# Kernel optimization log

Measured on AMD Instinct MI355X. Metric: run time of the kernel, lower is better.

The kernel has to match this reference:

```python
import jax, jax.numpy as jnp
import numpy as np

N, D, C, P = 4096, 512, 100, 64
EPS_COS = 1e-8   # torch cosine_similarity norm clamp
EPS_INV = 1e-5   # module's 1/(d + 1e-5)


def setup_inputs() -> dict:
    key = jax.random.key(0)
    k1, k2, k3, k4 = jax.random.split(key, 4)
    feats = jax.random.normal(k1, (N, D), dtype=jnp.float32)
    protos = jax.random.normal(k2, (C, P, D), dtype=jnp.float32)
    cls_ids = jax.random.randint(k3, (N,), 0, C)
    proto_labels = jax.random.randint(k4, (C, P), 0, 1000)
    return {"feats": feats, "protos": protos, "cls_ids": cls_ids,
            "proto_labels": proto_labels}


def reference(feats, protos, cls_ids, proto_labels):
    # Gather each box's class-conditional prototype set: [N, P, D]
    p = protos[cls_ids]
    pl = proto_labels[cls_ids]                       # [N, P]

    # cosine distance: 1 - f.p / (max(|f|,eps) * max(|p|,eps))
    dot = jnp.einsum('nd,npd->np', feats, p)         # [N, P]
    fnorm = jnp.maximum(jnp.linalg.norm(feats, axis=-1, keepdims=True), EPS_COS)
    pnorm = jnp.maximum(jnp.linalg.norm(p, axis=-1), EPS_COS)
    d_cos = 1.0 - dot / (fnorm * pnorm)

    diff = feats[:, None, :] - p                     # [N, P, D]
    d_l1 = jnp.mean(jnp.abs(diff), axis=-1)          # F.l1_loss (mean)
    d_l2 = jnp.mean(diff * diff, axis=-1)            # F.mse_loss (mean)

    dists = jnp.stack([d_cos, d_l1, d_l2], axis=1)   # [N, 3, P]
    probs = jax.nn.softmax(1.0 / (dists + EPS_INV), axis=-1).mean(axis=1)  # [N, P]

    idx = jnp.argmax(probs, axis=-1)                 # [N]
    labels = jnp.take_along_axis(pl, idx[:, None], axis=1)[:, 0]
    return labels, probs
```

## Files before the change

kernel.cpp:

```cpp
#include <hip/hip_runtime.h>

#define D 512
#define P 64
#define WPB 4
#define EPS_COS 1e-8f
#define EPS_INV 1e-5f

__device__ __forceinline__ float wave_sum(float v) {
#pragma unroll
    for (int m = 32; m >= 1; m >>= 1) v += __shfl_xor(v, m, 64);
    return v;
}

__global__ __launch_bounds__(256) void proto_norm_kernel(
    const float* __restrict__ protos, float* __restrict__ pp, int rows)
{
    const int lane = threadIdx.x & 63;
    const int wave = threadIdx.x >> 6;
    const int r = blockIdx.x * WPB + wave;
    if (r >= rows) return;
    const float* row = protos + (size_t)r * D;
    const float4 a = *(const float4*)(row + lane * 4);
    const float4 b = *(const float4*)(row + 256 + lane * 4);
    float s = a.x*a.x + a.y*a.y + a.z*a.z + a.w*a.w
            + b.x*b.x + b.y*b.y + b.z*b.z + b.w*b.w;
    s = wave_sum(s);
    if (lane == 0) pp[r] = s;
}

__global__ __launch_bounds__(WPB * 64) void proto_probs_kernel(
    const float* __restrict__ feats,
    const float* __restrict__ protos,
    const int*   __restrict__ cls_ids,
    const int*   __restrict__ proto_labels,
    const float* __restrict__ ppbuf,
    float* __restrict__ out,
    int N)
{
    const int lane = threadIdx.x & 63;
    const int wave = threadIdx.x >> 6;
    const int n = blockIdx.x * WPB + wave;
    if (n >= N) return;

    const int cls = cls_ids[n];
    const float* f  = feats  + (size_t)n * D;
    const float* pr = protos + (size_t)cls * (P * D);

    const float4 f0 = *(const float4*)(f + lane * 4);
    const float4 f1 = *(const float4*)(f + 256 + lane * 4);

    float ff = f0.x*f0.x + f0.y*f0.y + f0.z*f0.z + f0.w*f0.w
             + f1.x*f1.x + f1.y*f1.y + f1.z*f1.z + f1.w*f1.w;
    ff = wave_sum(ff);

    const int jsel = (lane >> 3) & 7;
    const int gown = lane & 7;
    const bool hi32 = (lane & 32) != 0;
    const bool hi16 = (lane & 16) != 0;
    const bool hi8  = (lane & 8)  != 0;

    float r_dot = 0.f, r_l1 = 0.f;

    for (int g = 0; g < 8; ++g) {
        float pd[8], pl[8];
#pragma unroll
        for (int j = 0; j < 8; ++j) {
            const float* row = pr + (size_t)(8 * g + j) * D;
            const float4 q0 = *(const float4*)(row + lane * 4);
            const float4 q1 = *(const float4*)(row + 256 + lane * 4);
            float dot, l1, t;
            dot  = f0.x*q0.x; t = f0.x - q0.x; l1  = fabsf(t);
            dot += f0.y*q0.y; t = f0.y - q0.y; l1 += fabsf(t);
            dot += f0.z*q0.z; t = f0.z - q0.z; l1 += fabsf(t);
            dot += f0.w*q0.w; t = f0.w - q0.w; l1 += fabsf(t);
            dot += f1.x*q1.x; t = f1.x - q1.x; l1 += fabsf(t);
            dot += f1.y*q1.y; t = f1.y - q1.y; l1 += fabsf(t);
            dot += f1.z*q1.z; t = f1.z - q1.z; l1 += fabsf(t);
            dot += f1.w*q1.w; t = f1.w - q1.w; l1 += fabsf(t);
            pd[j] = dot; pl[j] = l1;
        }
#pragma unroll
        for (int k = 0; k < 4; ++k) {
            const float sd = hi32 ? pd[k] : pd[k + 4];
            const float sl = hi32 ? pl[k] : pl[k + 4];
            const float rd = __shfl_xor(sd, 32, 64);
            const float rl = __shfl_xor(sl, 32, 64);
            pd[k] = (hi32 ? pd[k + 4] : pd[k]) + rd;
            pl[k] = (hi32 ? pl[k + 4] : pl[k]) + rl;
        }
#pragma unroll
        for (int k = 0; k < 2; ++k) {
            const float sd = hi16 ? pd[k] : pd[k + 2];
            const float sl = hi16 ? pl[k] : pl[k + 2];
            const float rd = __shfl_xor(sd, 16, 64);
            const float rl = __shfl_xor(sl, 16, 64);
            pd[k] = (hi16 ? pd[k + 2] : pd[k]) + rd;
            pl[k] = (hi16 ? pl[k + 2] : pl[k]) + rl;
        }
        {
            const float sd = hi8 ? pd[0] : pd[1];
            const float sl = hi8 ? pl[0] : pl[1];
            const float rd = __shfl_xor(sd, 8, 64);
            const float rl = __shfl_xor(sl, 8, 64);
            pd[0] = (hi8 ? pd[1] : pd[0]) + rd;
            pl[0] = (hi8 ? pl[1] : pl[0]) + rl;
        }
#pragma unroll
        for (int m = 4; m >= 1; m >>= 1) {
            pd[0] += __shfl_xor(pd[0], m, 64);
            pl[0] += __shfl_xor(pl[0], m, 64);
        }
        if (gown == g) { r_dot = pd[0]; r_l1 = pl[0]; }
    }

    const int myp = 8 * gown + jsel;
    const float s_pp = ppbuf[cls * P + myp];

    const float fnorm = fmaxf(sqrtf(ff),   EPS_COS);
    const float pnorm = fmaxf(sqrtf(s_pp), EPS_COS);
    const float d_cos = 1.0f - r_dot / (fnorm * pnorm);
    const float d_l1  = r_l1 * (1.0f / (float)D);
    const float d_l2  = (ff - 2.0f * r_dot + s_pp) * (1.0f / (float)D);

    float s[3];
    s[0] = 1.0f / (d_cos + EPS_INV);
    s[1] = 1.0f / (d_l1  + EPS_INV);
    s[2] = 1.0f / (d_l2  + EPS_INV);

    float prob = 0.f;
#pragma unroll
    for (int i = 0; i < 3; ++i) {
        float m = s[i];
#pragma unroll
        for (int w = 32; w >= 1; w >>= 1) m = fmaxf(m, __shfl_xor(m, w, 64));
        const float e = expf(s[i] - m);
        const float denom = wave_sum(e);
        prob += e / denom;
    }
    prob *= (1.0f / 3.0f);

    float best = prob;
    int   bidx = myp;
#pragma unroll
    for (int w = 32; w >= 1; w >>= 1) {
        const float ov = __shfl_xor(best, w, 64);
        const int   oi = __shfl_xor(bidx, w, 64);
        if (ov > best || (ov == best && oi < bidx)) { best = ov; bidx = oi; }
    }

    out[(size_t)N + (size_t)n * P + myp] = prob;
    if (lane == 0) {
        out[n] = (float)proto_labels[cls * P + bidx];
    }
}

extern "C" void kernel_launch(void* const* d_in, const int* in_sizes, int n_in,
                              void* d_out, int out_size, void* d_ws, size_t ws_size,
                              hipStream_t stream) {
    const float* feats        = (const float*)d_in[0];
    const float* protos       = (const float*)d_in[1];
    const int*   cls_ids      = (const int*)d_in[2];
    const int*   proto_labels = (const int*)d_in[3];
    float* out = (float*)d_out;
    float* pp  = (float*)d_ws;

    const int N    = in_sizes[2];
    const int rows = in_sizes[1] / D;

    proto_norm_kernel<<<(rows + WPB - 1) / WPB, WPB * 64, 0, stream>>>(
        protos, pp, rows);
    proto_probs_kernel<<<(N + WPB - 1) / WPB, WPB * 64, 0, stream>>>(
        feats, protos, cls_ids, proto_labels, pp, out, N);
}
```

Before: 104.6 us.

## Group boxes by class so each wave reuses prototype loads for two boxes

```diff
diff --git a/kernel.cpp b/kernel.cpp
--- a/kernel.cpp
+++ b/kernel.cpp
@@ -3,6 +3,8 @@
 #define D 512
 #define P 64
 #define WPB 4
+#define NB 2
+#define MAXC 256
 #define EPS_COS 1e-8f
 #define EPS_INV 1e-5f
 
@@ -28,30 +30,117 @@
     if (lane == 0) pp[r] = s;
 }
 
+__global__ __launch_bounds__(1024) void build_groups_kernel(
+    const int* __restrict__ cls_ids, int* __restrict__ slots,
+    int* __restrict__ gcount, int N, int C)
+{
+    __shared__ int cnt[MAXC], base[MAXC], fill[MAXC];
+    __shared__ int sG;
+    const int tid = threadIdx.x;
+    for (int c = tid; c < C; c += 1024) { cnt[c] = 0; fill[c] = 0; }
+    __syncthreads();
+    for (int n = tid; n < N; n += 1024) atomicAdd(&cnt[cls_ids[n]], 1);
+    __syncthreads();
+    if (tid == 0) {
+        int gb = 0;
+        for (int c = 0; c < C; ++c) { base[c] = gb; gb += (cnt[c] + NB - 1) / NB; }
+        sG = gb;
+        gcount[0] = gb;
+    }
+    __syncthreads();
+    const int G = sG;
+    for (int i = tid; i < G * NB; i += 1024) slots[i] = -1;
+    __syncthreads();
+    for (int n = tid; n < N; n += 1024) {
+        const int c = cls_ids[n];
+        const int p = atomicAdd(&fill[c], 1);
+        slots[base[c] * NB + p] = n;
+    }
+}
+
+__device__ __forceinline__ void box_epilogue(
+    float r_dot, float r_l1, float ff, float s_pp, int myp,
+    float& prob_o, int& bidx_o)
+{
+    const float fnorm = fmaxf(sqrtf(ff),   EPS_COS);
+    const float pnorm = fmaxf(sqrtf(s_pp), EPS_COS);
+    const float d_cos = 1.0f - r_dot / (fnorm * pnorm);
+    const float d_l1  = r_l1 * (1.0f / (float)D);
+    const float d_l2  = (ff - 2.0f * r_dot + s_pp) * (1.0f / (float)D);
+
+    float s[3];
+    s[0] = 1.0f / (d_cos + EPS_INV);
+    s[1] = 1.0f / (d_l1  + EPS_INV);
+    s[2] = 1.0f / (d_l2  + EPS_INV);
+
+    float prob = 0.f;
+#pragma unroll
+    for (int i = 0; i < 3; ++i) {
+        float m = s[i];
+#pragma unroll
+        for (int w = 32; w >= 1; w >>= 1) m = fmaxf(m, __shfl_xor(m, w, 64));
+        const float e = expf(s[i] - m);
+        const float denom = wave_sum(e);
+        prob += e / denom;
+    }
+    prob *= (1.0f / 3.0f);
+
+    float best = prob;
+    int   bidx = myp;
+#pragma unroll
+    for (int w = 32; w >= 1; w >>= 1) {
+        const float ov = __shfl_xor(best, w, 64);
+        const int   oi = __shfl_xor(bidx, w, 64);
+        if (ov > best || (ov == best && oi < bidx)) { best = ov; bidx = oi; }
+    }
+    prob_o = prob;
+    bidx_o = bidx;
+}
+
 __global__ __launch_bounds__(WPB * 64) void proto_probs_kernel(
     const float* __restrict__ feats,
     const float* __restrict__ protos,
     const int*   __restrict__ cls_ids,
     const int*   __restrict__ proto_labels,
     const float* __restrict__ ppbuf,
+    const int*   __restrict__ slots,
+    const int*   __restrict__ gcount,
     float* __restrict__ out,
     int N)
 {
     const int lane = threadIdx.x & 63;
     const int wave = threadIdx.x >> 6;
-    const int n = blockIdx.x * WPB + wave;
-    if (n >= N) return;
-
-    const int cls = cls_ids[n];
-    const float* f  = feats  + (size_t)n * D;
+
+    const int nb  = gridDim.x;
+    const int q   = nb >> 3, r = nb & 7;
+    const int xcd = blockIdx.x & 7, bix = blockIdx.x >> 3;
+    const int swz = (xcd < r ? xcd * (q + 1) : r * (q + 1) + (xcd - r) * q) + bix;
+
+    const int g = swz * WPB + wave;
+    if (g >= gcount[0]) return;
+
+    const int b0 = slots[g * NB + 0];
+    const int b1 = slots[g * NB + 1];
+    const bool v1 = (b1 >= 0);
+    const int n0 = b0;
+    const int n1 = v1 ? b1 : b0;
+
+    const int cls = cls_ids[n0];
+    const float* fa = feats  + (size_t)n0 * D;
+    const float* fb = feats  + (size_t)n1 * D;
     const float* pr = protos + (size_t)cls * (P * D);
 
-    const float4 f0 = *(const float4*)(f + lane * 4);
-    const float4 f1 = *(const float4*)(f + 256 + lane * 4);
-
-    float ff = f0.x*f0.x + f0.y*f0.y + f0.z*f0.z + f0.w*f0.w
-             + f1.x*f1.x + f1.y*f1.y + f1.z*f1.z + f1.w*f1.w;
-    ff = wave_sum(ff);
+    const float4 a0 = *(const float4*)(fa + lane * 4);
+    const float4 a1 = *(const float4*)(fa + 256 + lane * 4);
+    const float4 c0 = *(const float4*)(fb + lane * 4);
+    const float4 c1 = *(const float4*)(fb + 256 + lane * 4);
+
+    float ffa = a0.x*a0.x + a0.y*a0.y + a0.z*a0.z + a0.w*a0.w
+              + a1.x*a1.x + a1.y*a1.y + a1.z*a1.z + a1.w*a1.w;
+    float ffb = c0.x*c0.x + c0.y*c0.y + c0.z*c0.z + c0.w*c0.w
+              + c1.x*c1.x + c1.y*c1.y + c1.z*c1.z + c1.w*c1.w;
+    ffa = wave_sum(ffa);
+    ffb = wave_sum(ffb);
 
     const int jsel = (lane >> 3) & 7;
     const int gown = lane & 7;
@@ -59,98 +148,101 @@
     const bool hi16 = (lane & 16) != 0;
     const bool hi8  = (lane & 8)  != 0;
 
-    float r_dot = 0.f, r_l1 = 0.f;
-
-    for (int g = 0; g < 8; ++g) {
-        float pd[8], pl[8];
+    float rdA = 0.f, rlA = 0.f, rdB = 0.f, rlB = 0.f;
+
+    for (int gg = 0; gg < 8; ++gg) {
+        float pdA[8], plA[8], pdB[8], plB[8];
 #pragma unroll
         for (int j = 0; j < 8; ++j) {
-            const float* row = pr + (size_t)(8 * g + j) * D;
+            const float* row = pr + (size_t)(8 * gg + j) * D;
             const float4 q0 = *(const float4*)(row + lane * 4);
             const float4 q1 = *(const float4*)(row + 256 + lane * 4);
-            float dot, l1, t;
-            dot  = f0.x*q0.x; t = f0.x - q0.x; l1  = fabsf(t);
-            dot += f0.y*q0.y; t = f0.y - q0.y; l1 += fabsf(t);
-            dot += f0.z*q0.z; t = f0.z - q0.z; l1 += fabsf(t);
-            dot += f0.w*q0.w; t = f0.w - q0.w; l1 += fabsf(t);
-            dot += f1.x*q1.x; t = f1.x - q1.x; l1 += fabsf(t);
-            dot += f1.y*q1.y; t = f1.y - q1.y; l1 += fabsf(t);
-            dot += f1.z*q1.z; t = f1.z - q1.z; l1 += fabsf(t);
-            dot += f1.w*q1.w; t = f1.w - q1.w; l1 += fabsf(t);
-            pd[j] = dot; pl[j] = l1;
+            float dA, lA, dB, lB, t;
+            dA  = a0.x*q0.x; t = a0.x - q0.x; lA  = fabsf(t);
+            dA += a0.y*q0.y; t = a0.y - q0.y; lA += fabsf(t);
+            dA += a0.z*q0.z; t = a0.z - q0.z; lA += fabsf(t);
+            dA += a0.w*q0.w; t = a0.w - q0.w; lA += fabsf(t);
+            dA += a1.x*q1.x; t = a1.x - q1.x; lA += fabsf(t);
+            dA += a1.y*q1.y; t = a1.y - q1.y; lA += fabsf(t);
+            dA += a1.z*q1.z; t = a1.z - q1.z; lA += fabsf(t);
+            dA += a1.w*q1.w; t = a1.w - q1.w; lA += fabsf(t);
+            dB  = c0.x*q0.x; t = c0.x - q0.x; lB  = fabsf(t);
+            dB += c0.y*q0.y; t = c0.y - q0.y; lB += fabsf(t);
+            dB += c0.z*q0.z; t = c0.z - q0.z; lB += fabsf(t);
+            dB += c0.w*q0.w; t = c0.w - q0.w; lB += fabsf(t);
+            dB += c1.x*q1.x; t = c1.x - q1.x; lB += fabsf(t);
+            dB += c1.y*q1.y; t = c1.y - q1.y; lB += fabsf(t);
+            dB += c1.z*q1.z; t = c1.z - q1.z; lB += fabsf(t);
+            dB += c1.w*q1.w; t = c1.w - q1.w; lB += fabsf(t);
+            pdA[j] = dA; plA[j] = lA; pdB[j] = dB; plB[j] = lB;
         }
 #pragma unroll
         for (int k = 0; k < 4; ++k) {
-            const float sd = hi32 ? pd[k] : pd[k + 4];
-            const float sl = hi32 ? pl[k] : pl[k + 4];
-            const float rd = __shfl_xor(sd, 32, 64);
-            const float rl = __shfl_xor(sl, 32, 64);
-            pd[k] = (hi32 ? pd[k + 4] : pd[k]) + rd;
-            pl[k] = (hi32 ? pl[k + 4] : pl[k]) + rl;
+            const float sdA = hi32 ? pdA[k] : pdA[k + 4];
+            const float slA = hi32 ? plA[k] : plA[k + 4];
+            const float sdB = hi32 ? pdB[k] : pdB[k + 4];
+            const float slB = hi32 ? plB[k] : plB[k + 4];
+            const float rd0 = __shfl_xor(sdA, 32, 64);
+            const float rl0 = __shfl_xor(slA, 32, 64);
+            const float rd1 = __shfl_xor(sdB, 32, 64);
+            const float rl1 = __shfl_xor(slB, 32, 64);
+            pdA[k] = (hi32 ? pdA[k + 4] : pdA[k]) + rd0;
+            plA[k] = (hi32 ? plA[k + 4] : plA[k]) + rl0;
+            pdB[k] = (hi32 ? pdB[k + 4] : pdB[k]) + rd1;
+            plB[k] = (hi32 ? plB[k + 4] : plB[k]) + rl1;
         }
 #pragma unroll
         for (int k = 0; k < 2; ++k) {
-            const float sd = hi16 ? pd[k] : pd[k + 2];
-            const float sl = hi16 ? pl[k] : pl[k + 2];
-            const float rd = __shfl_xor(sd, 16, 64);
-            const float rl = __shfl_xor(sl, 16, 64);
-            pd[k] = (hi16 ? pd[k + 2] : pd[k]) + rd;
-            pl[k] = (hi16 ? pl[k + 2] : pl[k]) + rl;
+            const float sdA = hi16 ? pdA[k] : pdA[k + 2];
+            const float slA = hi16 ? plA[k] : plA[k + 2];
+            const float sdB = hi16 ? pdB[k] : pdB[k + 2];
+            const float slB = hi16 ? plB[k] : plB[k + 2];
+            const float rd0 = __shfl_xor(sdA, 16, 64);
+            const float rl0 = __shfl_xor(slA, 16, 64);
+            const float rd1 = __shfl_xor(sdB, 16, 64);
+            const float rl1 = __shfl_xor(slB, 16, 64);
+            pdA[k] = (hi16 ? pdA[k + 2] : pdA[k]) + rd0;
+            plA[k] = (hi16 ? plA[k + 2] : plA[k]) + rl0;
+            pdB[k] = (hi16 ? pdB[k + 2] : pdB[k]) + rd1;
+            plB[k] = (hi16 ? plB[k + 2] : plB[k]) + rl1;
         }
         {
-            const float sd = hi8 ? pd[0] : pd[1];
-            const float sl = hi8 ? pl[0] : pl[1];
-            const float rd = __shfl_xor(sd, 8, 64);
-            const float rl = __shfl_xor(sl, 8, 64);
-            pd[0] = (hi8 ? pd[1] : pd[0]) + rd;
-            pl[0] = (hi8 ? pl[1] : pl[0]) + rl;
+            const float sdA = hi8 ? pdA[0] : pdA[1];
+            const float slA = hi8 ? plA[0] : plA[1];
+            const float sdB = hi8 ? pdB[0] : pdB[1];
+            const float slB = hi8 ? plB[0] : plB[1];
+            const float rd0 = __shfl_xor(sdA, 8, 64);
+            const float rl0 = __shfl_xor(slA, 8, 64);
+            const float rd1 = __shfl_xor(sdB, 8, 64);
+            const float rl1 = __shfl_xor(slB, 8, 64);
+            pdA[0] = (hi8 ? pdA[1] : pdA[0]) + rd0;
+            plA[0] = (hi8 ? plA[1] : plA[0]) + rl0;
+            pdB[0] = (hi8 ? pdB[1] : pdB[0]) + rd1;
+            plB[0] = (hi8 ? plB[1] : plB[0]) + rl1;
         }
 #pragma unroll
         for (int m = 4; m >= 1; m >>= 1) {
-            pd[0] += __shfl_xor(pd[0], m, 64);
-            pl[0] += __shfl_xor(pl[0], m, 64);
-        }
-        if (gown == g) { r_dot = pd[0]; r_l1 = pl[0]; }
+            pdA[0] += __shfl_xor(pdA[0], m, 64);
+            plA[0] += __shfl_xor(plA[0], m, 64);
+            pdB[0] += __shfl_xor(pdB[0], m, 64);
+            plB[0] += __shfl_xor(plB[0], m, 64);
+        }
+        if (gown == gg) { rdA = pdA[0]; rlA = plA[0]; rdB = pdB[0]; rlB = plB[0]; }
     }
 
     const int myp = 8 * gown + jsel;
     const float s_pp = ppbuf[cls * P + myp];
 
-    const float fnorm = fmaxf(sqrtf(ff),   EPS_COS);
-    const float pnorm = fmaxf(sqrtf(s_pp), EPS_COS);
-    const float d_cos = 1.0f - r_dot / (fnorm * pnorm);
-    const float d_l1  = r_l1 * (1.0f / (float)D);
-    const float d_l2  = (ff - 2.0f * r_dot + s_pp) * (1.0f / (float)D);
-
-    float s[3];
-    s[0] = 1.0f / (d_cos + EPS_INV);
-    s[1] = 1.0f / (d_l1  + EPS_INV);
-    s[2] = 1.0f / (d_l2  + EPS_INV);
-
-    float prob = 0.f;
-#pragma unroll
-    for (int i = 0; i < 3; ++i) {
-        float m = s[i];
-#pragma unroll
-        for (int w = 32; w >= 1; w >>= 1) m = fmaxf(m, __shfl_xor(m, w, 64));
-        const float e = expf(s[i] - m);
-        const float denom = wave_sum(e);
-        prob += e / denom;
-    }
-    prob *= (1.0f / 3.0f);
-
-    float best = prob;
-    int   bidx = myp;
-#pragma unroll
-    for (int w = 32; w >= 1; w >>= 1) {
-        const float ov = __shfl_xor(best, w, 64);
-        const int   oi = __shfl_xor(bidx, w, 64);
-        if (ov > best || (ov == best && oi < bidx)) { best = ov; bidx = oi; }
-    }
-
-    out[(size_t)N + (size_t)n * P + myp] = prob;
-    if (lane == 0) {
-        out[n] = (float)proto_labels[cls * P + bidx];
+    float probA; int bidxA;
+    box_epilogue(rdA, rlA, ffa, s_pp, myp, probA, bidxA);
+    out[(size_t)N + (size_t)n0 * P + myp] = probA;
+    if (lane == 0) out[n0] = (float)proto_labels[cls * P + bidxA];
+
+    if (v1) {
+        float probB; int bidxB;
+        box_epilogue(rdB, rlB, ffb, s_pp, myp, probB, bidxB);
+        out[(size_t)N + (size_t)n1 * P + myp] = probB;
+        if (lane == 0) out[n1] = (float)proto_labels[cls * P + bidxB];
     }
 }
 
@@ -162,13 +254,21 @@
     const int*   cls_ids      = (const int*)d_in[2];
     const int*   proto_labels = (const int*)d_in[3];
     float* out = (float*)d_out;
-    float* pp  = (float*)d_ws;
 
     const int N    = in_sizes[2];
     const int rows = in_sizes[1] / D;
+    const int C    = rows / P;
+
+    float* pp     = (float*)d_ws;
+    int*   gcount = (int*)((char*)d_ws + (size_t)rows * sizeof(float));
+    int*   slots  = gcount + 1;
+
+    const int Gmax    = (N + C * (NB - 1)) / NB;
+    const int mblocks = (Gmax + WPB - 1) / WPB;
 
     proto_norm_kernel<<<(rows + WPB - 1) / WPB, WPB * 64, 0, stream>>>(
         protos, pp, rows);
-    proto_probs_kernel<<<(N + WPB - 1) / WPB, WPB * 64, 0, stream>>>(
-        feats, protos, cls_ids, proto_labels, pp, out, N);
-}
+    build_groups_kernel<<<1, 1024, 0, stream>>>(cls_ids, slots, gcount, N, C);
+    proto_probs_kernel<<<mblocks, WPB * 64, 0, stream>>>(
+        feats, protos, cls_ids, proto_labels, pp, slots, gcount, out, N);
+}
```

Measured after the change: 119.2 us. +14.0%, slower.

## Group boxes by class in pairs, transpose prototypes, one prototype per lane

Applied to the files above, without the earlier changes.

```diff
diff --git a/kernel.cpp b/kernel.cpp
--- a/kernel.cpp
+++ b/kernel.cpp
@@ -1,8 +1,11 @@
 #include <hip/hip_runtime.h>
 
 #define D 512
+#define D4 (D / 4)
 #define P 64
 #define WPB 4
+#define NB 2
+#define MAXC 256
 #define EPS_COS 1e-8f
 #define EPS_INV 1e-5f
 
@@ -12,145 +15,183 @@
     return v;
 }
 
-__global__ __launch_bounds__(256) void proto_norm_kernel(
-    const float* __restrict__ protos, float* __restrict__ pp, int rows)
+__global__ __launch_bounds__(256) void prep_kernel(
+    const float* __restrict__ protos, float* __restrict__ pp,
+    float* __restrict__ protosT, int rows,
+    const int* __restrict__ cls_ids, int* __restrict__ slots,
+    int* __restrict__ gcount, int N, int C, int normBlocks, int trBlocks)
 {
+    const int bid  = blockIdx.x;
     const int lane = threadIdx.x & 63;
     const int wave = threadIdx.x >> 6;
-    const int r = blockIdx.x * WPB + wave;
-    if (r >= rows) return;
-    const float* row = protos + (size_t)r * D;
-    const float4 a = *(const float4*)(row + lane * 4);
-    const float4 b = *(const float4*)(row + 256 + lane * 4);
-    float s = a.x*a.x + a.y*a.y + a.z*a.z + a.w*a.w
-            + b.x*b.x + b.y*b.y + b.z*b.z + b.w*b.w;
-    s = wave_sum(s);
-    if (lane == 0) pp[r] = s;
+
+    if (bid < normBlocks) {
+        const int r = bid * WPB + wave;
+        if (r >= rows) return;
+        const float* row = protos + (size_t)r * D;
+        const float4 a = *(const float4*)(row + lane * 4);
+        const float4 b = *(const float4*)(row + 256 + lane * 4);
+        float s = a.x*a.x + a.y*a.y + a.z*a.z + a.w*a.w
+                + b.x*b.x + b.y*b.y + b.z*b.z + b.w*b.w;
+        s = wave_sum(s);
+        if (lane == 0) pp[r] = s;
+        return;
+    }
+
+    if (bid < normBlocks + trBlocks) {
+        const int idx = (bid - normBlocks) * WPB + wave;
+        if (idx >= C * D4) return;
+        const int c  = idx >> 7;
+        const int d4 = idx & (D4 - 1);
+        const float4 v = *(const float4*)(protos + (size_t)(c * P + lane) * D + 4 * d4);
+        *(float4*)(protosT + ((size_t)(c * D4 + d4) * P + lane) * 4) = v;
+        return;
+    }
+
+    __shared__ int cnt[MAXC], bas[MAXC], fil[MAXC];
+    __shared__ int sv[256];
+    const int tid = threadIdx.x;
+    for (int c = tid; c < MAXC; c += 256) { cnt[c] = 0; fil[c] = 0; }
+    __syncthreads();
+    for (int n = tid; n < N; n += 256) atomicAdd(&cnt[cls_ids[n]], 1);
+    __syncthreads();
+    int v = 0;
+    if (tid < C) v = (cnt[tid] + NB - 1) / NB;
+    sv[tid] = v;
+    __syncthreads();
+#pragma unroll
+    for (int off = 1; off < 256; off <<= 1) {
+        const int t = (tid >= off) ? sv[tid - off] : 0;
+        __syncthreads();
+        sv[tid] += t;
+        __syncthreads();
+    }
+    const int G = sv[255];
+    if (tid < C) bas[tid] = sv[tid] - v;
+    if (tid == 0) gcount[0] = G;
+    __syncthreads();
+    for (int i = tid; i < G * NB; i += 256) slots[i] = -1;
+    __syncthreads();
+    for (int n = tid; n < N; n += 256) {
+        const int c = cls_ids[n];
+        const int p = atomicAdd(&fil[c], 1);
+        slots[bas[c] * NB + p] = n;
+    }
+}
+
+__device__ __forceinline__ void box_epilogue(
+    float r_dot, float r_l1, float ff, float s_pp, int myp,
+    float& prob_o, int& bidx_o)
+{
+    const float fnorm = fmaxf(sqrtf(ff),   EPS_COS);
+    const float pnorm = fmaxf(sqrtf(s_pp), EPS_COS);
+    const float d_cos = 1.0f - r_dot / (fnorm * pnorm);
+    const float d_l1  = r_l1 * (1.0f / (float)D);
+    const float d_l2  = (ff - 2.0f * r_dot + s_pp) * (1.0f / (float)D);
+
+    float s[3];
+    s[0] = 1.0f / (d_cos + EPS_INV);
+    s[1] = 1.0f / (d_l1  + EPS_INV);
+    s[2] = 1.0f / (d_l2  + EPS_INV);
+
+    float prob = 0.f;
+#pragma unroll
+    for (int i = 0; i < 3; ++i) {
+        float m = s[i];
+#pragma unroll
+        for (int w = 32; w >= 1; w >>= 1) m = fmaxf(m, __shfl_xor(m, w, 64));
+        const float e = expf(s[i] - m);
+        const float denom = wave_sum(e);
+        prob += e / denom;
+    }
+    prob *= (1.0f / 3.0f);
+
+    float best = prob;
+    int   bidx = myp;
+#pragma unroll
+    for (int w = 32; w >= 1; w >>= 1) {
+        const float ov = __shfl_xor(best, w, 64);
+        const int   oi = __shfl_xor(bidx, w, 64);
+        if (ov > best || (ov == best && oi < bidx)) { best = ov; bidx = oi; }
+    }
+    prob_o = prob;
+    bidx_o = bidx;
 }
 
 __global__ __launch_bounds__(WPB * 64) void proto_probs_kernel(
     const float* __restrict__ feats,
-    const float* __restrict__ protos,
+    const float* __restrict__ protosT,
     const int*   __restrict__ cls_ids,
     const int*   __restrict__ proto_labels,
     const float* __restrict__ ppbuf,
+    const int*   __restrict__ slots,
+    const int*   __restrict__ gcount,
     float* __restrict__ out,
     int N)
 {
     const int lane = threadIdx.x & 63;
     const int wave = threadIdx.x >> 6;
-    const int n = blockIdx.x * WPB + wave;
-    if (n >= N) return;
-
-    const int cls = cls_ids[n];
-    const float* f  = feats  + (size_t)n * D;
-    const float* pr = protos + (size_t)cls * (P * D);
-
-    const float4 f0 = *(const float4*)(f + lane * 4);
-    const float4 f1 = *(const float4*)(f + 256 + lane * 4);
-
-    float ff = f0.x*f0.x + f0.y*f0.y + f0.z*f0.z + f0.w*f0.w
-             + f1.x*f1.x + f1.y*f1.y + f1.z*f1.z + f1.w*f1.w;
-    ff = wave_sum(ff);
-
-    const int jsel = (lane >> 3) & 7;
-    const int gown = lane & 7;
-    const bool hi32 = (lane & 32) != 0;
-    const bool hi16 = (lane & 16) != 0;
-    const bool hi8  = (lane & 8)  != 0;
-
-    float r_dot = 0.f, r_l1 = 0.f;
-
-    for (int g = 0; g < 8; ++g) {
-        float pd[8], pl[8];
-#pragma unroll
-        for (int j = 0; j < 8; ++j) {
-            const float* row = pr + (size_t)(8 * g + j) * D;
-            const float4 q0 = *(const float4*)(row + lane * 4);
-            const float4 q1 = *(const float4*)(row + 256 + lane * 4);
-            float dot, l1, t;
-            dot  = f0.x*q0.x; t = f0.x - q0.x; l1  = fabsf(t);
-            dot += f0.y*q0.y; t = f0.y - q0.y; l1 += fabsf(t);
-            dot += f0.z*q0.z; t = f0.z - q0.z; l1 += fabsf(t);
-            dot += f0.w*q0.w; t = f0.w - q0.w; l1 += fabsf(t);
-            dot += f1.x*q1.x; t = f1.x - q1.x; l1 += fabsf(t);
-            dot += f1.y*q1.y; t = f1.y - q1.y; l1 += fabsf(t);
-            dot += f1.z*q1.z; t = f1.z - q1.z; l1 += fabsf(t);
-            dot += f1.w*q1.w; t = f1.w - q1.w; l1 += fabsf(t);
-            pd[j] = dot; pl[j] = l1;
-        }
-#pragma unroll
-        for (int k = 0; k < 4; ++k) {
-            const float sd = hi32 ? pd[k] : pd[k + 4];
-            const float sl = hi32 ? pl[k] : pl[k + 4];
-            const float rd = __shfl_xor(sd, 32, 64);
-            const float rl = __shfl_xor(sl, 32, 64);
-            pd[k] = (hi32 ? pd[k + 4] : pd[k]) + rd;
-            pl[k] = (hi32 ? pl[k + 4] : pl[k]) + rl;
-        }
-#pragma unroll
-        for (int k = 0; k < 2; ++k) {
-            const float sd = hi16 ? pd[k] : pd[k + 2];
-            const float sl = hi16 ? pl[k] : pl[k + 2];
-            const float rd = __shfl_xor(sd, 16, 64);
-            const float rl = __shfl_xor(sl, 16, 64);
-            pd[k] = (hi16 ? pd[k + 2] : pd[k]) + rd;
-            pl[k] = (hi16 ? pl[k + 2] : pl[k]) + rl;
-        }
-        {
-            const float sd = hi8 ? pd[0] : pd[1];
-            const float sl = hi8 ? pl[0] : pl[1];
-            const float rd = __shfl_xor(sd, 8, 64);
-            const float rl = __shfl_xor(sl, 8, 64);
-            pd[0] = (hi8 ? pd[1] : pd[0]) + rd;
-            pl[0] = (hi8 ? pl[1] : pl[0]) + rl;
-        }
-#pragma unroll
-        for (int m = 4; m >= 1; m >>= 1) {
-            pd[0] += __shfl_xor(pd[0], m, 64);
-            pl[0] += __shfl_xor(pl[0], m, 64);
-        }
-        if (gown == g) { r_dot = pd[0]; r_l1 = pl[0]; }
-    }
-
-    const int myp = 8 * gown + jsel;
-    const float s_pp = ppbuf[cls * P + myp];
-
-    const float fnorm = fmaxf(sqrtf(ff),   EPS_COS);
-    const float pnorm = fmaxf(sqrtf(s_pp), EPS_COS);
-    const float d_cos = 1.0f - r_dot / (fnorm * pnorm);
-    const float d_l1  = r_l1 * (1.0f / (float)D);
-    const float d_l2  = (ff - 2.0f * r_dot + s_pp) * (1.0f / (float)D);
-
-    float s[3];
-    s[0] = 1.0f / (d_cos + EPS_INV);
-    s[1] = 1.0f / (d_l1  + EPS_INV);
-    s[2] = 1.0f / (d_l2  + EPS_INV);
-
-    float prob = 0.f;
-#pragma unroll
-    for (int i = 0; i < 3; ++i) {
-        float m = s[i];
-#pragma unroll
-        for (int w = 32; w >= 1; w >>= 1) m = fmaxf(m, __shfl_xor(m, w, 64));
-        const float e = expf(s[i] - m);
-        const float denom = wave_sum(e);
-        prob += e / denom;
-    }
-    prob *= (1.0f / 3.0f);
-
-    float best = prob;
-    int   bidx = myp;
-#pragma unroll
-    for (int w = 32; w >= 1; w >>= 1) {
-        const float ov = __shfl_xor(best, w, 64);
-        const int   oi = __shfl_xor(bidx, w, 64);
-        if (ov > best || (ov == best && oi < bidx)) { best = ov; bidx = oi; }
-    }
-
-    out[(size_t)N + (size_t)n * P + myp] = prob;
-    if (lane == 0) {
-        out[n] = (float)proto_labels[cls * P + bidx];
+
+    const int nbk = gridDim.x;
+    const int q   = nbk >> 3, r = nbk & 7;
+    const int xcd = blockIdx.x & 7, bix = blockIdx.x >> 3;
+    const int swz = (xcd < r ? xcd * (q + 1) : r * (q + 1) + (xcd - r) * q) + bix;
+
+    const int g = swz * WPB + wave;
+    if (g >= gcount[0]) return;
+
+    const int b0 = __builtin_amdgcn_readfirstlane(slots[NB * g]);
+    const int b1 = __builtin_amdgcn_readfirstlane(slots[NB * g + 1]);
+    const bool v1 = (b1 >= 0);
+    const int n0 = b0;
+    const int n1 = v1 ? b1 : b0;
+    const int cls = __builtin_amdgcn_readfirstlane(cls_ids[n0]);
+
+    const float* fA = feats   + (size_t)n0 * D;
+    const float* fB = feats   + (size_t)n1 * D;
+    const float* pT = protosT + (size_t)cls * (D4 * P * 4);
+
+    float ffA, ffB;
+    {
+        const float4 a0 = *(const float4*)(fA + lane * 4);
+        const float4 a1 = *(const float4*)(fA + 256 + lane * 4);
+        ffA = wave_sum(a0.x*a0.x + a0.y*a0.y + a0.z*a0.z + a0.w*a0.w
+                     + a1.x*a1.x + a1.y*a1.y + a1.z*a1.z + a1.w*a1.w);
+        const float4 c0 = *(const float4*)(fB + lane * 4);
+        const float4 c1 = *(const float4*)(fB + 256 + lane * 4);
+        ffB = wave_sum(c0.x*c0.x + c0.y*c0.y + c0.z*c0.z + c0.w*c0.w
+                     + c1.x*c1.x + c1.y*c1.y + c1.z*c1.z + c1.w*c1.w);
+    }
+
+    float dotA = 0.f, l1A = 0.f, dotB = 0.f, l1B = 0.f;
+#pragma unroll 8
+    for (int d4 = 0; d4 < D4; ++d4) {
+        const float4 qv = *(const float4*)(pT + (size_t)(d4 * P + lane) * 4);
+        const float4 av = *(const float4*)(fA + 4 * d4);
+        const float4 bv = *(const float4*)(fB + 4 * d4);
+        float t;
+        dotA += av.x*qv.x; t = av.x - qv.x; l1A += fabsf(t);
+        dotA += av.y*qv.y; t = av.y - qv.y; l1A += fabsf(t);
+        dotA += av.z*qv.z; t = av.z - qv.z; l1A += fabsf(t);
+        dotA += av.w*qv.w; t = av.w - qv.w; l1A += fabsf(t);
+        dotB += bv.x*qv.x; t = bv.x - qv.x; l1B += fabsf(t);
+        dotB += bv.y*qv.y; t = bv.y - qv.y; l1B += fabsf(t);
+        dotB += bv.z*qv.z; t = bv.z - qv.z; l1B += fabsf(t);
+        dotB += bv.w*qv.w; t = bv.w - qv.w; l1B += fabsf(t);
+    }
+
+    const float s_pp = ppbuf[cls * P + lane];
+
+    float probA; int bidxA;
+    box_epilogue(dotA, l1A, ffA, s_pp, lane, probA, bidxA);
+    out[(size_t)N + (size_t)n0 * P + lane] = probA;
+    if (lane == 0) out[n0] = (float)proto_labels[cls * P + bidxA];
+
+    if (v1) {
+        float probB; int bidxB;
+        box_epilogue(dotB, l1B, ffB, s_pp, lane, probB, bidxB);
+        out[(size_t)N + (size_t)n1 * P + lane] = probB;
+        if (lane == 0) out[n1] = (float)proto_labels[cls * P + bidxB];
     }
 }
 
@@ -162,13 +203,26 @@
     const int*   cls_ids      = (const int*)d_in[2];
     const int*   proto_labels = (const int*)d_in[3];
     float* out = (float*)d_out;
-    float* pp  = (float*)d_ws;
 
     const int N    = in_sizes[2];
     const int rows = in_sizes[1] / D;
-
-    proto_norm_kernel<<<(rows + WPB - 1) / WPB, WPB * 64, 0, stream>>>(
-        protos, pp, rows);
-    proto_probs_kernel<<<(N + WPB - 1) / WPB, WPB * 64, 0, stream>>>(
-        feats, protos, cls_ids, proto_labels, pp, out, N);
-}
+    const int C    = rows / P;
+    const int Gmax = (N + C * (NB - 1)) / NB;
+
+    float* pp     = (float*)d_ws;
+    int*   gcount = (int*)(pp + rows);
+    int*   slots  = gcount + 1;
+    size_t off = (size_t)rows * 4 + 4 + (size_t)Gmax * NB * 4;
+    off = (off + 255) & ~(size_t)255;
+    float* protosT = (float*)((char*)d_ws + off);
+
+    const int normBlocks = (rows + WPB - 1) / WPB;
+    const int trBlocks   = (C * D4 + WPB - 1) / WPB;
+    const int mainBlocks = (Gmax + WPB - 1) / WPB;
+
+    prep_kernel<<<normBlocks + trBlocks + 1, 256, 0, stream>>>(
+        protos, pp, protosT, rows, cls_ids, slots, gcount, N, C,
+        normBlocks, trBlocks);
+    proto_probs_kernel<<<mainBlocks, WPB * 64, 0, stream>>>(
+        feats, protosT, cls_ids, proto_labels, pp, slots, gcount, out, N);
+}
```

Result: slower. 137.3 us (+31.2%).
